# Optimization experiments

Hardware: AMD Instinct MI355X
Metric: run time of the kernel (lower is better)

## Reference

```python
import jax, jax.numpy as jnp
import numpy as np

B, C, S, H, W = 2, 128, 64, 128, 512
MID = 32
EPS = 1e-5


def layer_norm(x, g, b):
    m = jnp.mean(x, axis=-1, keepdims=True)
    v = jnp.var(x, axis=-1, keepdims=True)
    return (x - m) / jnp.sqrt(v + EPS) * g + b


def generate_y_for_attn(s, y, u):
    # y: [B, Cy, H, W], u: [B, s, s] int indices into W (clamped)
    b, cy, h, w = y.shape
    u = jnp.clip(u, 0, w - 1)
    yr = y.reshape(b, cy * h, w)
    idx = u.reshape(b, s * s)
    g = jax.vmap(lambda m, i: m[:, i])(yr, idx)          # [B, Cy*H, s^2]
    return g.reshape(b, cy, h, s * s).transpose(0, 3, 2, 1)  # [B, s^2, H, Cy]


def setup_inputs():
    key = jax.random.key(0)
    ks = jax.random.split(key, 10)
    lim = 1.0 / np.sqrt(C)
    return {
        "sat_x": jax.random.normal(ks[0], (B, C, S, S), jnp.float32),
        "grd_x": jax.random.normal(ks[1], (B, C, H, W), jnp.float32),
        "grd_height": jax.random.normal(ks[2], (B, 1, H, W), jnp.float32),
        "u": jax.random.randint(ks[3], (B, S, S), 0, W, jnp.int32),
        "ln_q_g": jnp.ones((C,), jnp.float32),
        "ln_q_b": jnp.zeros((C,), jnp.float32),
        "wq": jax.random.uniform(ks[4], (C, MID), jnp.float32, -lim, lim),
        "bq": jax.random.uniform(ks[5], (MID,), jnp.float32, -lim, lim),
        "ln_k_g": jnp.ones((C,), jnp.float32),
        "ln_k_b": jnp.zeros((C,), jnp.float32),
        "wk": jax.random.uniform(ks[6], (C, MID), jnp.float32, -lim, lim),
        "bk": jax.random.uniform(ks[7], (MID,), jnp.float32, -lim, lim),
    }


def reference(sat_x, grd_x, grd_height, u, ln_q_g, ln_q_b, wq, bq, ln_k_g, ln_k_b, wk, bk):
    b, c, s, _ = sat_x.shape
    scale = MID ** (-0.5)
    y_attn = generate_y_for_attn(s, grd_x, u)        # [B, S^2, H, C]
    v_attn = generate_y_for_attn(s, grd_height, u)   # [B, S^2, H, 1]
    x = sat_x.reshape(b, c, s * s).transpose(0, 2, 1)  # [B, M, C]
    q = layer_norm(x, ln_q_g, ln_q_b) @ wq + bq        # [B, M, 32]
    k = layer_norm(y_attn, ln_k_g, ln_k_b) @ wk + bk   # [B, M, H, 32]
    dot = scale * jnp.einsum("bmd,bmnd->bmn", q, k)    # [B, M, H]
    att = jax.nn.softmax(dot, axis=-1)
    a = jnp.sum(att[..., None] * v_attn, axis=-2)      # [B, M, 1]
    return a.transpose(0, 2, 1).reshape(b, 1, s, s)
```

## Files before the change

### kernel.cpp

```cpp
#include <hip/hip_runtime.h>
#include <math.h>

#define B_   2
#define C_   128
#define S_   64
#define H_   128
#define W_   512
#define M_   (S_ * S_)
#define MID_ 32
#define EPS_ 1e-5f
#define CAP_ 192

#define KBLK (B_ * H_ * (W_ / 64))
#define QBLK (B_ * (M_ / 64))

typedef __attribute__((ext_vector_type(8))) short short8;
typedef __attribute__((ext_vector_type(4))) float floatx4;

__global__ __launch_bounds__(256) void prep_kernel(
    const float* __restrict__ ln_k_g, const float* __restrict__ ln_k_b,
    const float* __restrict__ wk, const float* __restrict__ bk,
    const float* __restrict__ ln_q_g, const float* __restrict__ ln_q_b,
    const float* __restrict__ wq, const float* __restrict__ bq,
    float* __restrict__ prepbuf,
    short* __restrict__ wfrag,
    int* __restrict__ counts)
{
    const int tid = threadIdx.x;
    const int blk = blockIdx.x;
    const float* g    = blk ? ln_q_g : ln_k_g;
    const float* bl   = blk ? ln_q_b : ln_k_b;
    const float* wt   = blk ? wq     : wk;
    const float* bias = blk ? bq     : bk;

    __shared__ float pa[256], pb[256];

    float a = 0.f, c2 = 0.f;
#pragma unroll
    for (int k = 0; k < 16; ++k) {
        const int idx = tid + 256 * k;
        const float wv = wt[idx];
        const int c = idx >> 5;
        a  = fmaf(g[c],  wv, a);
        c2 = fmaf(bl[c], wv, c2);
    }
    pa[tid] = a; pb[tid] = c2;

    if (blk == 0) {
        ((int4*)counts)[tid] = make_int4(0, 0, 0, 0);
    }
    __syncthreads();

    if (tid < 32) {
        float s = 0.f, t = 0.f;
#pragma unroll
        for (int r = 0; r < 8; ++r) { s += pa[tid + 32 * r]; t += pb[tid + 32 * r]; }
        prepbuf[blk * 64 + tid]      = s;
        prepbuf[blk * 64 + 32 + tid] = t + bias[tid];
    }

    short* whiT = wfrag + blk * 8192;
    short* wloT = whiT + 4096;
#pragma unroll
    for (int e = 0; e < 16; ++e) {
        const int idx = tid * 16 + e;
        const int i    = idx & 7;
        const int ln   = (idx >> 3) & 63;
        const int kk   = (idx >> 9) & 3;
        const int jt   = idx >> 11;
        const int c = kk * 32 + (ln >> 4) * 8 + i;
        const int j = jt * 16 + (ln & 15);
        const float wp = g[c] * wt[c * MID_ + j];
        const unsigned bbits = __float_as_uint(wp);
        const unsigned hb = bbits & 0xFFFF0000u;
        whiT[idx] = (short)(hb >> 16);
        const float r = wp - __uint_as_float(hb);
        wloT[idx] = (short)(__float_as_uint(r) >> 16);
    }
}

__global__ __launch_bounds__(64) void proj_kernel(
    const float* __restrict__ grd_x,
    const float* __restrict__ sat_x,
    const float* __restrict__ prepbuf,
    const short* __restrict__ wfrag,
    float* __restrict__ kw,
    float* __restrict__ qv)
{
    const int lane = threadIdx.x;
    const int quad = lane >> 4;
    const int l16  = lane & 15;
    const int blk  = blockIdx.x;
    const bool is_k = (blk < KBLK);

    int b, h = 0, pos0;
    const float* xcol;
    size_t xstr;
    if (is_k) {
        const int wchunk = blk & 7;
        h    = (blk >> 3) & (H_ - 1);
        b    = blk >> 10;
        pos0 = wchunk * 64;
        xcol = grd_x + ((size_t)b * C_ * H_ + h) * W_ + pos0;
        xstr = (size_t)H_ * W_;
    } else {
        const int qblk = blk - KBLK;
        b    = qblk >> 6;
        pos0 = (qblk & 63) * 64;
        xcol = sat_x + (size_t)b * C_ * M_ + pos0;
        xstr = (size_t)M_;
    }

    const short* whiT = wfrag + (is_k ? 0 : 8192);
    const short* wloT = whiT + 4096;
    short8 ahi[2][4], alo[2][4];
#pragma unroll
    for (int jt = 0; jt < 2; ++jt)
#pragma unroll
        for (int kk = 0; kk < 4; ++kk) {
            const int off = ((jt * 4 + kk) * 64 + lane) * 8;
            ahi[jt][kk] = *(const short8*)(whiT + off);
            alo[jt][kk] = *(const short8*)(wloT + off);
        }

    const int setoff = is_k ? 0 : 64;
    const float4 gw0 = *(const float4*)(prepbuf + setoff + quad * 4);
    const float4 bw0 = *(const float4*)(prepbuf + setoff + 32 + quad * 4);
    const float4 gw1 = *(const float4*)(prepbuf + setoff + 16 + quad * 4);
    const float4 bw1 = *(const float4*)(prepbuf + setoff + 48 + quad * 4);

#pragma unroll
    for (int pt = 0; pt < 4; ++pt) {
        const float* xp = xcol + (size_t)(quad * 8) * xstr + pt * 16 + l16;
        float xv[32];
#pragma unroll
        for (int kk = 0; kk < 4; ++kk)
#pragma unroll
            for (int i = 0; i < 8; ++i)
                xv[kk * 8 + i] = xp[(size_t)(kk * 32 + i) * xstr];

        floatx4 acc0 = {0.f, 0.f, 0.f, 0.f};
        floatx4 acc1 = {0.f, 0.f, 0.f, 0.f};
        float p1 = 0.f, p2 = 0.f;

#pragma unroll
        for (int kk = 0; kk < 4; ++kk) {
            union { short8 v; unsigned u[4]; } bhi, blo;
#pragma unroll
            for (int e = 0; e < 4; ++e) {
                const float x0 = xv[kk * 8 + 2 * e];
                const float x1 = xv[kk * 8 + 2 * e + 1];
                p1 += x0 + x1;
                p2 = fmaf(x0, x0, p2);
                p2 = fmaf(x1, x1, p2);
                const unsigned b0 = __float_as_uint(x0);
                const unsigned b1 = __float_as_uint(x1);
                bhi.u[e] = (b1 & 0xFFFF0000u) | (b0 >> 16);
                const float r0 = x0 - __uint_as_float(b0 & 0xFFFF0000u);
                const float r1 = x1 - __uint_as_float(b1 & 0xFFFF0000u);
                blo.u[e] = (__float_as_uint(r1) & 0xFFFF0000u) |
                           (__float_as_uint(r0) >> 16);
            }
            acc0 = __builtin_amdgcn_mfma_f32_16x16x32_bf16(ahi[0][kk], bhi.v, acc0, 0, 0, 0);
            acc1 = __builtin_amdgcn_mfma_f32_16x16x32_bf16(ahi[1][kk], bhi.v, acc1, 0, 0, 0);
            acc0 = __builtin_amdgcn_mfma_f32_16x16x32_bf16(ahi[0][kk], blo.v, acc0, 0, 0, 0);
            acc1 = __builtin_amdgcn_mfma_f32_16x16x32_bf16(ahi[1][kk], blo.v, acc1, 0, 0, 0);
            acc0 = __builtin_amdgcn_mfma_f32_16x16x32_bf16(alo[0][kk], bhi.v, acc0, 0, 0, 0);
            acc1 = __builtin_amdgcn_mfma_f32_16x16x32_bf16(alo[1][kk], bhi.v, acc1, 0, 0, 0);
        }

        p1 += __shfl_xor(p1, 16, 64);
        p1 += __shfl_xor(p1, 32, 64);
        p2 += __shfl_xor(p2, 16, 64);
        p2 += __shfl_xor(p2, 32, 64);
        const float mean = p1 * (1.f / C_);
        const float rstd = rsqrtf(fmaf(-mean, mean, p2 * (1.f / C_)) + EPS_);

        const int pos = pos0 + pt * 16 + l16;
        float* orow;
        if (is_k) orow = kw + (((size_t)b * W_ + pos) * H_ + h) * MID_;
        else      orow = qv + ((size_t)b * M_ + pos) * MID_;

        orow[quad * 4 + 0]      = fmaf(rstd, fmaf(-mean, gw0.x, acc0[0]), bw0.x);
        orow[quad * 4 + 1]      = fmaf(rstd, fmaf(-mean, gw0.y, acc0[1]), bw0.y);
        orow[quad * 4 + 2]      = fmaf(rstd, fmaf(-mean, gw0.z, acc0[2]), bw0.z);
        orow[quad * 4 + 3]      = fmaf(rstd, fmaf(-mean, gw0.w, acc0[3]), bw0.w);
        orow[16 + quad * 4 + 0] = fmaf(rstd, fmaf(-mean, gw1.x, acc1[0]), bw1.x);
        orow[16 + quad * 4 + 1] = fmaf(rstd, fmaf(-mean, gw1.y, acc1[1]), bw1.y);
        orow[16 + quad * 4 + 2] = fmaf(rstd, fmaf(-mean, gw1.z, acc1[2]), bw1.z);
        orow[16 + quad * 4 + 3] = fmaf(rstd, fmaf(-mean, gw1.w, acc1[3]), bw1.w);
    }
}

__global__ __launch_bounds__(256) void count_kernel(
    const int*   __restrict__ u,
    const float* __restrict__ qv,
    const float* __restrict__ kw,
    const float* __restrict__ gh,
    int* __restrict__ counts,
    int* __restrict__ bucket,
    float* __restrict__ out)
{
    const int bm = blockIdx.x * 256 + threadIdx.x;
    const int b  = bm >> 12;
    int w = u[bm];
    w = min(max(w, 0), W_ - 1);
    const int bw  = b * W_ + w;
    const int pos = atomicAdd(&counts[bw], 1);
    if (pos < CAP_) {
        bucket[bw * CAP_ + pos] = bm;
    } else {
        const float* qr = qv + (size_t)bm * MID_;
        const float* kr = kw + (size_t)bw * H_ * MID_;
        float mx = -1e30f, s = 0.f, sv = 0.f;
        for (int h = 0; h < H_; ++h) {
            float d = 0.f;
            for (int j = 0; j < MID_; ++j) d = fmaf(qr[j], kr[h * MID_ + j], d);
            d *= 0.17677669529663687f;
            const float nm   = fmaxf(mx, d);
            const float corr = __expf(mx - nm);
            const float e    = __expf(d - nm);
            s  = fmaf(s,  corr, e);
            sv = fmaf(sv, corr, e * gh[((size_t)b * H_ + h) * W_ + w]);
            mx = nm;
        }
        out[bm] = sv / s;
    }
}

__global__ __launch_bounds__(256) void battn_kernel(
    const float* __restrict__ qv,
    const float* __restrict__ kw,
    const float* __restrict__ gh,
    const int*   __restrict__ counts,
    const int*   __restrict__ bucket,
    float* __restrict__ out)
{
    const int blk = blockIdx.x;
    const int n   = min(counts[blk], CAP_);
    const int tid  = threadIdx.x;
    const int lane = tid & 63;
    const int wv   = __builtin_amdgcn_readfirstlane(tid >> 6);
    if (wv >= n) return;

    const int b = blk >> 9;
    const int w = blk & (W_ - 1);

    const float4* k4 = (const float4*)(kw + (size_t)blk * H_ * MID_);
    float4 ka[8], kb[8];
#pragma unroll
    for (int j = 0; j < 8; ++j) ka[j] = k4[lane * 8 + j];
#pragma unroll
    for (int j = 0; j < 8; ++j) kb[j] = k4[(lane + 64) * 8 + j];

    const float v0 = gh[((size_t)b * H_ + lane) * W_ + w];
    const float v1 = gh[((size_t)b * H_ + lane + 64) * W_ + w];

    const int* bkt = bucket + (size_t)blk * CAP_;
    const float sc = 0.17677669529663687f;

    for (int i = wv; i < n; i += 4) {
        const int bm = bkt[i];
        const float* qr = qv + (size_t)bm * MID_;
        float sq[MID_];
#pragma unroll
        for (int j = 0; j < MID_; ++j) sq[j] = qr[j];

        float d0 = 0.f, d1 = 0.f;
#pragma unroll
        for (int j = 0; j < 8; ++j) {
            d0 = fmaf(sq[j * 4 + 0], ka[j].x, d0);
            d0 = fmaf(sq[j * 4 + 1], ka[j].y, d0);
            d0 = fmaf(sq[j * 4 + 2], ka[j].z, d0);
            d0 = fmaf(sq[j * 4 + 3], ka[j].w, d0);
            d1 = fmaf(sq[j * 4 + 0], kb[j].x, d1);
            d1 = fmaf(sq[j * 4 + 1], kb[j].y, d1);
            d1 = fmaf(sq[j * 4 + 2], kb[j].z, d1);
            d1 = fmaf(sq[j * 4 + 3], kb[j].w, d1);
        }
        d0 *= sc; d1 *= sc;

        float mx = fmaxf(d0, d1);
#pragma unroll
        for (int o = 32; o > 0; o >>= 1) mx = fmaxf(mx, __shfl_xor(mx, o, 64));

        const float e0 = __expf(d0 - mx);
        const float e1 = __expf(d1 - mx);
        float s   = e0 + e1;
        float svv = fmaf(e0, v0, e1 * v1);
#pragma unroll
        for (int o = 32; o > 0; o >>= 1) {
            s   += __shfl_xor(s,   o, 64);
            svv += __shfl_xor(svv, o, 64);
        }

        if (lane == 0) out[bm] = svv / s;
    }
}

extern "C" void kernel_launch(void* const* d_in, const int* in_sizes, int n_in,
                              void* d_out, int out_size, void* d_ws, size_t ws_size,
                              hipStream_t stream) {
    const float* sat_x      = (const float*)d_in[0];
    const float* grd_x      = (const float*)d_in[1];
    const float* grd_height = (const float*)d_in[2];
    const int*   u          = (const int*)d_in[3];
    const float* ln_q_g     = (const float*)d_in[4];
    const float* ln_q_b     = (const float*)d_in[5];
    const float* wq         = (const float*)d_in[6];
    const float* bq         = (const float*)d_in[7];
    const float* ln_k_g     = (const float*)d_in[8];
    const float* ln_k_b     = (const float*)d_in[9];
    const float* wk         = (const float*)d_in[10];
    const float* bk         = (const float*)d_in[11];

    float* out = (float*)d_out;

    char* ws = (char*)d_ws;
    float* kw      = (float*)ws;
    float* q       = (float*)(ws + (size_t)16 * 1024 * 1024);
    int*   counts  = (int*)  (ws + (size_t)17 * 1024 * 1024);
    int*   bucket  = counts + B_ * W_;
    float* prepbuf = (float*)(ws + (size_t)18 * 1024 * 1024);
    short* wfrag   = (short*)(ws + (size_t)18 * 1024 * 1024 + 4096);

    prep_kernel<<<2, 256, 0, stream>>>(
        ln_k_g, ln_k_b, wk, bk, ln_q_g, ln_q_b, wq, bq, prepbuf, wfrag, counts);
    proj_kernel<<<KBLK + QBLK, 64, 0, stream>>>(
        grd_x, sat_x, prepbuf, wfrag, kw, q);
    count_kernel<<<(B_ * M_) / 256, 256, 0, stream>>>(
        u, q, kw, grd_height, counts, bucket, out);
    battn_kernel<<<B_ * W_, 256, 0, stream>>>(
        q, kw, grd_height, counts, bucket, out);
}
```

Measured before the change: 146.4 us.

## Fuse bucket counting into projection kernel and move overflow to attention blocks

Removes the separate count kernel. The q-projection blocks now bucket each query by its clamped u index. Overflow queries beyond the bucket capacity go into a global list, which a few extra attention blocks process with wave-parallel softmax instead of the serial per-thread loop. The projection kernel also changes from one 64-thread wave looping over four 16-column tiles to four waves each handling one tile, and it writes outputs as float4 stores. This cuts one launch and improves parallelism, but adds atomics inside the projection kernel and loses reuse of the weight fragments across tiles within a wave.

```diff
diff --git a/kernel.cpp b/kernel.cpp
--- a/kernel.cpp
+++ b/kernel.cpp
@@ -13,6 +13,7 @@
 
 #define KBLK (B_ * H_ * (W_ / 64))
 #define QBLK (B_ * (M_ / 64))
+#define OBLK 4
 
 typedef __attribute__((ext_vector_type(8))) short short8;
 typedef __attribute__((ext_vector_type(4))) float floatx4;
@@ -24,7 +25,8 @@
     const float* __restrict__ wq, const float* __restrict__ bq,
     float* __restrict__ prepbuf,
     short* __restrict__ wfrag,
-    int* __restrict__ counts)
+    int* __restrict__ counts,
+    int* __restrict__ ocount)
 {
     const int tid = threadIdx.x;
     const int blk = blockIdx.x;
@@ -48,6 +50,7 @@
 
     if (blk == 0) {
         ((int4*)counts)[tid] = make_int4(0, 0, 0, 0);
+        if (tid == 0) *ocount = 0;
     }
     __syncthreads();
 
@@ -79,15 +82,22 @@
     }
 }
 
-__global__ __launch_bounds__(64) void proj_kernel(
+__global__ __launch_bounds__(256) void proj_kernel(
     const float* __restrict__ grd_x,
     const float* __restrict__ sat_x,
     const float* __restrict__ prepbuf,
     const short* __restrict__ wfrag,
+    const int*   __restrict__ u,
     float* __restrict__ kw,
-    float* __restrict__ qv)
+    float* __restrict__ qv,
+    int* __restrict__ counts,
+    int* __restrict__ bucket,
+    int* __restrict__ ocount,
+    int* __restrict__ olist)
 {
-    const int lane = threadIdx.x;
+    const int tid  = threadIdx.x;
+    const int lane = tid & 63;
+    const int wv   = __builtin_amdgcn_readfirstlane(tid >> 6);
     const int quad = lane >> 4;
     const int l16  = lane & 15;
     const int blk  = blockIdx.x;
@@ -110,6 +120,15 @@
         xcol = sat_x + (size_t)b * C_ * M_ + pos0;
         xstr = (size_t)M_;
     }
+    const int pos = pos0 + wv * 16 + l16;
+
+    const float* xp = xcol + (size_t)(quad * 8) * xstr + wv * 16 + l16;
+    float xv[32];
+#pragma unroll
+    for (int kk = 0; kk < 4; ++kk)
+#pragma unroll
+        for (int i = 0; i < 8; ++i)
+            xv[kk * 8 + i] = xp[(size_t)(kk * 32 + i) * xstr];
 
     const short* whiT = wfrag + (is_k ? 0 : 8192);
     const short* wloT = whiT + 4096;
@@ -129,102 +148,67 @@
     const float4 gw1 = *(const float4*)(prepbuf + setoff + 16 + quad * 4);
     const float4 bw1 = *(const float4*)(prepbuf + setoff + 48 + quad * 4);
 
-#pragma unroll
-    for (int pt = 0; pt < 4; ++pt) {
-        const float* xp = xcol + (size_t)(quad * 8) * xstr + pt * 16 + l16;
-        float xv[32];
-#pragma unroll
-        for (int kk = 0; kk < 4; ++kk)
-#pragma unroll
-            for (int i = 0; i < 8; ++i)
-                xv[kk * 8 + i] = xp[(size_t)(kk * 32 + i) * xstr];
-
-        floatx4 acc0 = {0.f, 0.f, 0.f, 0.f};
-        floatx4 acc1 = {0.f, 0.f, 0.f, 0.f};
-        float p1 = 0.f, p2 = 0.f;
-
-#pragma unroll
-        for (int kk = 0; kk < 4; ++kk) {
-            union { short8 v; unsigned u[4]; } bhi, blo;
-#pragma unroll
-            for (int e = 0; e < 4; ++e) {
-                const float x0 = xv[kk * 8 + 2 * e];
-                const float x1 = xv[kk * 8 + 2 * e + 1];
-                p1 += x0 + x1;
-                p2 = fmaf(x0, x0, p2);
-                p2 = fmaf(x1, x1, p2);
-                const unsigned b0 = __float_as_uint(x0);
-                const unsigned b1 = __float_as_uint(x1);
-                bhi.u[e] = (b1 & 0xFFFF0000u) | (b0 >> 16);
-                const float r0 = x0 - __uint_as_float(b0 & 0xFFFF0000u);
-                const float r1 = x1 - __uint_as_float(b1 & 0xFFFF0000u);
-                blo.u[e] = (__float_as_uint(r1) & 0xFFFF0000u) |
-                           (__float_as_uint(r0) >> 16);
-            }
-            acc0 = __builtin_amdgcn_mfma_f32_16x16x32_bf16(ahi[0][kk], bhi.v, acc0, 0, 0, 0);
-            acc1 = __builtin_amdgcn_mfma_f32_16x16x32_bf16(ahi[1][kk], bhi.v, acc1, 0, 0, 0);
-            acc0 = __builtin_amdgcn_mfma_f32_16x16x32_bf16(ahi[0][kk], blo.v, acc0, 0, 0, 0);
-            acc1 = __builtin_amdgcn_mfma_f32_16x16x32_bf16(ahi[1][kk], blo.v, acc1, 0, 0, 0);
-            acc0 = __builtin_amdgcn_mfma_f32_16x16x32_bf16(alo[0][kk], bhi.v, acc0, 0, 0, 0);
-            acc1 = __builtin_amdgcn_mfma_f32_16x16x32_bf16(alo[1][kk], bhi.v, acc1, 0, 0, 0);
-        }
-
-        p1 += __shfl_xor(p1, 16, 64);
-        p1 += __shfl_xor(p1, 32, 64);
-        p2 += __shfl_xor(p2, 16, 64);
-        p2 += __shfl_xor(p2, 32, 64);
-        const float mean = p1 * (1.f / C_);
-        const float rstd = rsqrtf(fmaf(-mean, mean, p2 * (1.f / C_)) + EPS_);
-
-        const int pos = pos0 + pt * 16 + l16;
-        float* orow;
-        if (is_k) orow = kw + (((size_t)b * W_ + pos) * H_ + h) * MID_;
-        else      orow = qv + ((size_t)b * M_ + pos) * MID_;
-
-        orow[quad * 4 + 0]      = fmaf(rstd, fmaf(-mean, gw0.x, acc0[0]), bw0.x);
-        orow[quad * 4 + 1]      = fmaf(rstd, fmaf(-mean, gw0.y, acc0[1]), bw0.y);
-        orow[quad * 4 + 2]      = fmaf(rstd, fmaf(-mean, gw0.z, acc0[2]), bw0.z);
-        orow[quad * 4 + 3]      = fmaf(rstd, fmaf(-mean, gw0.w, acc0[3]), bw0.w);
-        orow[16 + quad * 4 + 0] = fmaf(rstd, fmaf(-mean, gw1.x, acc1[0]), bw1.x);
-        orow[16 + quad * 4 + 1] = fmaf(rstd, fmaf(-mean, gw1.y, acc1[1]), bw1.y);
-        orow[16 + quad * 4 + 2] = fmaf(rstd, fmaf(-mean, gw1.z, acc1[2]), bw1.z);
-        orow[16 + quad * 4 + 3] = fmaf(rstd, fmaf(-mean, gw1.w, acc1[3]), bw1.w);
-    }
-}
-
-__global__ __launch_bounds__(256) void count_kernel(
-    const int*   __restrict__ u,
-    const float* __restrict__ qv,
-    const float* __restrict__ kw,
-    const float* __restrict__ gh,
-    int* __restrict__ counts,
-    int* __restrict__ bucket,
-    float* __restrict__ out)
-{
-    const int bm = blockIdx.x * 256 + threadIdx.x;
-    const int b  = bm >> 12;
-    int w = u[bm];
-    w = min(max(w, 0), W_ - 1);
-    const int bw  = b * W_ + w;
-    const int pos = atomicAdd(&counts[bw], 1);
-    if (pos < CAP_) {
-        bucket[bw * CAP_ + pos] = bm;
-    } else {
-        const float* qr = qv + (size_t)bm * MID_;
-        const float* kr = kw + (size_t)bw * H_ * MID_;
-        float mx = -1e30f, s = 0.f, sv = 0.f;
-        for (int h = 0; h < H_; ++h) {
-            float d = 0.f;
-            for (int j = 0; j < MID_; ++j) d = fmaf(qr[j], kr[h * MID_ + j], d);
-            d *= 0.17677669529663687f;
-            const float nm   = fmaxf(mx, d);
-            const float corr = __expf(mx - nm);
-            const float e    = __expf(d - nm);
-            s  = fmaf(s,  corr, e);
-            sv = fmaf(sv, corr, e * gh[((size_t)b * H_ + h) * W_ + w]);
-            mx = nm;
-        }
-        out[bm] = sv / s;
+    floatx4 acc0 = {0.f, 0.f, 0.f, 0.f};
+    floatx4 acc1 = {0.f, 0.f, 0.f, 0.f};
+    float p1 = 0.f, p2 = 0.f;
+
+#pragma unroll
+    for (int kk = 0; kk < 4; ++kk) {
+        union { short8 v; unsigned u[4]; } bhi, blo;
+#pragma unroll
+        for (int e = 0; e < 4; ++e) {
+            const float x0 = xv[kk * 8 + 2 * e];
+            const float x1 = xv[kk * 8 + 2 * e + 1];
+            p1 += x0 + x1;
+            p2 = fmaf(x0, x0, p2);
+            p2 = fmaf(x1, x1, p2);
+            const unsigned b0 = __float_as_uint(x0);
+            const unsigned b1 = __float_as_uint(x1);
+            bhi.u[e] = (b1 & 0xFFFF0000u) | (b0 >> 16);
+            const float r0 = x0 - __uint_as_float(b0 & 0xFFFF0000u);
+            const float r1 = x1 - __uint_as_float(b1 & 0xFFFF0000u);
+            blo.u[e] = (__float_as_uint(r1) & 0xFFFF0000u) |
+                       (__float_as_uint(r0) >> 16);
+        }
+        acc0 = __builtin_amdgcn_mfma_f32_16x16x32_bf16(ahi[0][kk], bhi.v, acc0, 0, 0, 0);
+        acc1 = __builtin_amdgcn_mfma_f32_16x16x32_bf16(ahi[1][kk], bhi.v, acc1, 0, 0, 0);
+        acc0 = __builtin_amdgcn_mfma_f32_16x16x32_bf16(ahi[0][kk], blo.v, acc0, 0, 0, 0);
+        acc1 = __builtin_amdgcn_mfma_f32_16x16x32_bf16(ahi[1][kk], blo.v, acc1, 0, 0, 0);
+        acc0 = __builtin_amdgcn_mfma_f32_16x16x32_bf16(alo[0][kk], bhi.v, acc0, 0, 0, 0);
+        acc1 = __builtin_amdgcn_mfma_f32_16x16x32_bf16(alo[1][kk], bhi.v, acc1, 0, 0, 0);
+    }
+
+    p1 += __shfl_xor(p1, 16, 64);
+    p1 += __shfl_xor(p1, 32, 64);
+    p2 += __shfl_xor(p2, 16, 64);
+    p2 += __shfl_xor(p2, 32, 64);
+    const float mean = p1 * (1.f / C_);
+    const float rstd = rsqrtf(fmaf(-mean, mean, p2 * (1.f / C_)) + EPS_);
+
+    float* orow;
+    if (is_k) orow = kw + (((size_t)b * W_ + pos) * H_ + h) * MID_;
+    else      orow = qv + ((size_t)b * M_ + pos) * MID_;
+
+    float4 o0, o1;
+    o0.x = fmaf(rstd, fmaf(-mean, gw0.x, acc0[0]), bw0.x);
+    o0.y = fmaf(rstd, fmaf(-mean, gw0.y, acc0[1]), bw0.y);
+    o0.z = fmaf(rstd, fmaf(-mean, gw0.z, acc0[2]), bw0.z);
+    o0.w = fmaf(rstd, fmaf(-mean, gw0.w, acc0[3]), bw0.w);
+    o1.x = fmaf(rstd, fmaf(-mean, gw1.x, acc1[0]), bw1.x);
+    o1.y = fmaf(rstd, fmaf(-mean, gw1.y, acc1[1]), bw1.y);
+    o1.z = fmaf(rstd, fmaf(-mean, gw1.z, acc1[2]), bw1.z);
+    o1.w = fmaf(rstd, fmaf(-mean, gw1.w, acc1[3]), bw1.w);
+    *(float4*)(orow + quad * 4)      = o0;
+    *(float4*)(orow + 16 + quad * 4) = o1;
+
+    if (!is_k && quad == 0) {
+        const int bm = b * M_ + pos;
+        int w = u[bm];
+        w = min(max(w, 0), W_ - 1);
+        const int bw = b * W_ + w;
+        const int p = atomicAdd(&counts[bw], 1);
+        if (p < CAP_) bucket[bw * CAP_ + p] = bm;
+        else          olist[atomicAdd(ocount, 1)] = bm;
     }
 }
 
@@ -232,15 +216,63 @@
     const float* __restrict__ qv,
     const float* __restrict__ kw,
     const float* __restrict__ gh,
+    const int*   __restrict__ u,
     const int*   __restrict__ counts,
     const int*   __restrict__ bucket,
+    const int*   __restrict__ ocount,
+    const int*   __restrict__ olist,
     float* __restrict__ out)
 {
-    const int blk = blockIdx.x;
-    const int n   = min(counts[blk], CAP_);
+    const int blk  = blockIdx.x;
     const int tid  = threadIdx.x;
     const int lane = tid & 63;
     const int wv   = __builtin_amdgcn_readfirstlane(tid >> 6);
+    const float sc = 0.17677669529663687f;
+
+    if (blk >= B_ * W_) {
+        const int nof = min(*ocount, B_ * M_);
+        const int gwv = (blk - B_ * W_) * 4 + wv;
+        for (int i = gwv; i < nof; i += OBLK * 4) {
+            const int bm = olist[i];
+            const int b  = bm >> 12;
+            int w = u[bm];
+            w = min(max(w, 0), W_ - 1);
+            const float4* k4 = (const float4*)(kw + ((size_t)b * W_ + w) * H_ * MID_);
+            const float* qr = qv + (size_t)bm * MID_;
+            float sq[MID_];
+#pragma unroll
+            for (int j = 0; j < MID_; ++j) sq[j] = qr[j];
+            float d0 = 0.f, d1 = 0.f;
+#pragma unroll
+            for (int j = 0; j < 8; ++j) {
+                const float4 ka = k4[lane * 8 + j];
+                const float4 kb = k4[(lane + 64) * 8 + j];
+                d0 = fmaf(sq[j*4+0], ka.x, d0); d0 = fmaf(sq[j*4+1], ka.y, d0);
+                d0 = fmaf(sq[j*4+2], ka.z, d0); d0 = fmaf(sq[j*4+3], ka.w, d0);
+                d1 = fmaf(sq[j*4+0], kb.x, d1); d1 = fmaf(sq[j*4+1], kb.y, d1);
+                d1 = fmaf(sq[j*4+2], kb.z, d1); d1 = fmaf(sq[j*4+3], kb.w, d1);
+            }
+            d0 *= sc; d1 *= sc;
+            float mx = fmaxf(d0, d1);
+#pragma unroll
+            for (int o = 32; o > 0; o >>= 1) mx = fmaxf(mx, __shfl_xor(mx, o, 64));
+            const float v0 = gh[((size_t)b * H_ + lane) * W_ + w];
+            const float v1 = gh[((size_t)b * H_ + lane + 64) * W_ + w];
+            const float e0 = __expf(d0 - mx);
+            const float e1 = __expf(d1 - mx);
+            float s   = e0 + e1;
+            float svv = fmaf(e0, v0, e1 * v1);
+#pragma unroll
+            for (int o = 32; o > 0; o >>= 1) {
+                s   += __shfl_xor(s,   o, 64);
+                svv += __shfl_xor(svv, o, 64);
+            }
+            if (lane == 0) out[bm] = svv / s;
+        }
+        return;
+    }
+
+    const int n = min(counts[blk], CAP_);
     if (wv >= n) return;
 
     const int b = blk >> 9;
@@ -257,7 +289,6 @@
     const float v1 = gh[((size_t)b * H_ + lane + 64) * W_ + w];
 
     const int* bkt = bucket + (size_t)blk * CAP_;
-    const float sc = 0.17677669529663687f;
 
     for (int i = wv; i < n; i += 4) {
         const int bm = bkt[i];
@@ -320,16 +351,17 @@
     float* kw      = (float*)ws;
     float* q       = (float*)(ws + (size_t)16 * 1024 * 1024);
     int*   counts  = (int*)  (ws + (size_t)17 * 1024 * 1024);
-    int*   bucket  = counts + B_ * W_;
+    int*   ocount  = (int*)  (ws + (size_t)17 * 1024 * 1024 + 4096);
+    int*   bucket  = (int*)  (ws + (size_t)17 * 1024 * 1024 + 8192);
+    int*   olist   = bucket + B_ * W_ * CAP_;
     float* prepbuf = (float*)(ws + (size_t)18 * 1024 * 1024);
     short* wfrag   = (short*)(ws + (size_t)18 * 1024 * 1024 + 4096);
 
     prep_kernel<<<2, 256, 0, stream>>>(
-        ln_k_g, ln_k_b, wk, bk, ln_q_g, ln_q_b, wq, bq, prepbuf, wfrag, counts);
-    proj_kernel<<<KBLK + QBLK, 64, 0, stream>>>(
-        grd_x, sat_x, prepbuf, wfrag, kw, q);
-    count_kernel<<<(B_ * M_) / 256, 256, 0, stream>>>(
-        u, q, kw, grd_height, counts, bucket, out);
-    battn_kernel<<<B_ * W_, 256, 0, stream>>>(
-        q, kw, grd_height, counts, bucket, out);
+        ln_k_g, ln_k_b, wk, bk, ln_q_g, ln_q_b, wq, bq,
+        prepbuf, wfrag, counts, ocount);
+    proj_kernel<<<KBLK + QBLK, 256, 0, stream>>>(
+        grd_x, sat_x, prepbuf, wfrag, u, kw, q, counts, bucket, ocount, olist);
+    battn_kernel<<<B_ * W_ + OBLK, 256, 0, stream>>>(
+        q, kw, grd_height, u, counts, bucket, ocount, olist, out);
 }
```

Result: no change. 144.6 us (-1.2%).
